# Optimization experiments

Hardware: AMD Instinct MI355X
Metric: run time of the kernel (lower is better)

The kernel has to match this reference:

```python
import jax, jax.numpy as jnp
import numpy as np

LN_EPS = 1e-3   # keras LayerNormalization default epsilon
EPS = 1e-5      # module's self.eps
QB = 128.0      # 2**(bits-1) with bits=8


def ste_round(x):
    # straight-through round: forward = round(x), backward = identity
    return x + jax.lax.stop_gradient(jnp.round(x) - x)


def setup_inputs() -> dict:
    key = jax.random.key(0)
    k1, k2 = jax.random.split(key)
    x = jax.random.normal(k1, (4, 8192, 1024), dtype=jnp.float32)
    weight = jax.random.normal(k2, (1024, 1024), dtype=jnp.float32) * 0.02
    ln_gamma = jnp.ones((1024,), dtype=jnp.float32)
    ln_beta = jnp.zeros((1024,), dtype=jnp.float32)
    return {"x": x, "weight": weight, "ln_gamma": ln_gamma, "ln_beta": ln_beta}


def reference(x, weight, ln_gamma, ln_beta):
    # LayerNorm over last axis (keras defaults: eps=1e-3, learnable scale/center)
    mu = jnp.mean(x, axis=-1, keepdims=True)
    var = jnp.var(x, axis=-1, keepdims=True)
    xn = (x - mu) * jax.lax.rsqrt(var + LN_EPS) * ln_gamma + ln_beta

    # 1.58-bit weight ternarization with STE round
    beta = jnp.mean(jnp.abs(weight))                     # per-tensor scale
    w_q = jnp.clip(ste_round(weight / (beta + EPS)), -1.0, 1.0)

    # activation quantization (flg_before_linear=True branch)
    gamma = jnp.max(jnp.abs(xn))                         # per-tensor absmax
    xq = jnp.clip(xn * QB / gamma, -QB + EPS, QB - EPS)

    # quantized matmul + fused rescale
    y = jnp.einsum('bsd,du->bsu', xq, w_q)
    return y * (gamma * beta / QB)
```

## Files before the change

kernel.cpp:

```cpp
#include <hip/hip_runtime.h>
#include <hip/hip_bf16.h>
#include <stdint.h>


#define M_ROWS 32768
#define KDIM 1024
#define NDIM 1024

typedef int   v4i  __attribute__((ext_vector_type(4)));
typedef int   v16i __attribute__((ext_vector_type(16)));

__device__ __forceinline__ void async16(const void* g, void* l) {
    __builtin_amdgcn_global_load_lds((const __attribute__((address_space(1))) uint32_t*)g,
                                     (__attribute__((address_space(3))) uint32_t*)l,
                                     16, 0, 0);
}

__global__ __launch_bounds__(256) void absum_k(const float* __restrict__ w,
                                               float* __restrict__ partials) {
    int idx = blockIdx.x * 256 + threadIdx.x;
    float4 v = ((const float4*)w)[idx];
    float s = fabsf(v.x) + fabsf(v.y) + fabsf(v.z) + fabsf(v.w);
    #pragma unroll
    for (int o = 32; o; o >>= 1) s += __shfl_xor(s, o);
    __shared__ float p[4];
    if ((threadIdx.x & 63) == 0) p[threadIdx.x >> 6] = s;
    __syncthreads();
    if (threadIdx.x == 0) partials[blockIdx.x] = p[0] + p[1] + p[2] + p[3];
}

__global__ __launch_bounds__(256) void quant_k(const float* __restrict__ w,
                                               const float* __restrict__ partials,
                                               char* __restrict__ wqT,
                                               float* __restrict__ wsum) {
    int t = threadIdx.x;
    float s = partials[t] + partials[t + 256] + partials[t + 512] + partials[t + 768];
    #pragma unroll
    for (int o = 32; o; o >>= 1) s += __shfl_xor(s, o);
    __shared__ float ps[4];
    if ((t & 63) == 0) ps[t >> 6] = s;
    __syncthreads();
    float total = ps[0] + ps[1] + ps[2] + ps[3];
    if (blockIdx.x == 0 && t == 0) wsum[0] = total;
    float beta = total * (1.0f / 1048576.0f);
    float inv  = 1.0f / (beta + 1e-5f);

    __shared__ char sT[64 * 80];
    int k0 = (blockIdx.x >> 4) * 64, n0 = (blockIdx.x & 15) * 64;
    int n_l = t & 63;
    #pragma unroll
    for (int r = 0; r < 16; ++r) {
        int k_l = (t >> 6) * 16 + r;
        float q = rintf(w[(size_t)(k0 + k_l) * NDIM + n0 + n_l] * inv);
        q = fminf(1.0f, fmaxf(-1.0f, q));
        sT[n_l * 80 + k_l] = (char)(int)q;
    }
    __syncthreads();
    int nn = t >> 2, c = t & 3;
    v4i val = *(const v4i*)&sT[nn * 80 + c * 16];
    *(v4i*)&wqT[(size_t)(n0 + nn) * KDIM + k0 + c * 16] = val;
}

__global__ __launch_bounds__(256) void ln_q_k(const float* __restrict__ x,
                                              const float* __restrict__ g,
                                              const float* __restrict__ b,
                                              char* __restrict__ xq,
                                              float* __restrict__ rscale) {
    int tid = threadIdx.x;
    int lane = tid & 63;
    int row = blockIdx.x * 4 + (tid >> 6);
    const float4* xr = (const float4*)(x + (size_t)row * KDIM);
    float4 v[4];
    #pragma unroll
    for (int j = 0; j < 4; ++j) v[j] = xr[lane + 64 * j];
    float s = 0.f, ss = 0.f;
    #pragma unroll
    for (int j = 0; j < 4; ++j) {
        s  += v[j].x + v[j].y + v[j].z + v[j].w;
        ss += v[j].x * v[j].x + v[j].y * v[j].y + v[j].z * v[j].z + v[j].w * v[j].w;
    }
    #pragma unroll
    for (int o = 32; o; o >>= 1) { s += __shfl_xor(s, o); ss += __shfl_xor(ss, o); }
    float mu  = s * (1.0f / 1024.0f);
    float var = ss * (1.0f / 1024.0f) - mu * mu;
    float rs  = rsqrtf(var + 1e-3f);
    float xn[16];
    float mx = 0.f;
    #pragma unroll
    for (int j = 0; j < 4; ++j) {
        int p = lane + 64 * j;
        float4 gg = ((const float4*)g)[p];
        float4 bb = ((const float4*)b)[p];
        xn[4*j+0] = (v[j].x - mu) * rs * gg.x + bb.x;
        xn[4*j+1] = (v[j].y - mu) * rs * gg.y + bb.y;
        xn[4*j+2] = (v[j].z - mu) * rs * gg.z + bb.z;
        xn[4*j+3] = (v[j].w - mu) * rs * gg.w + bb.w;
        #pragma unroll
        for (int e = 0; e < 4; ++e) mx = fmaxf(mx, fabsf(xn[4*j+e]));
    }
    #pragma unroll
    for (int o = 32; o; o >>= 1) mx = fmaxf(mx, __shfl_xor(mx, o));
    mx = fmaxf(mx, 1e-20f);
    float scl = mx * (1.0f / 127.0f);
    float inv = 127.0f / mx;
    if (lane == 0) rscale[row] = scl;
    #pragma unroll
    for (int j = 0; j < 4; ++j) {
        char4 c;
        c.x = (char)(int)rintf(xn[4*j+0] * inv);
        c.y = (char)(int)rintf(xn[4*j+1] * inv);
        c.z = (char)(int)rintf(xn[4*j+2] * inv);
        c.w = (char)(int)rintf(xn[4*j+3] * inv);
        *(char4*)(xq + (size_t)row * KDIM + (lane + 64 * j) * 4) = c;
    }
}

__global__ __launch_bounds__(256) void gemm_k(const char* __restrict__ A,
                                              const char* __restrict__ B,
                                              const float* __restrict__ wsum,
                                              const float* __restrict__ rscale,
                                              float* __restrict__ out) {
    __shared__ char sA[128 * 128];
    __shared__ char sB[128 * 128];
    int tid = threadIdx.x;
    int w = tid >> 6, lane = tid & 63;
    int half = lane >> 5, l31 = lane & 31;
    int wm = w & 1, wn = w >> 1;
    int xcd   = blockIdx.x & 7;
    int local = blockIdx.x >> 3;
    int bm0 = (xcd * 32 + (local >> 3)) * 128;
    int bn0 = (local & 7) * 128;

    v16i acc[2][2] = {};

    int r_sub = lane >> 3;
    int p     = lane & 7;

    for (int kt = 0; kt < 8; ++kt) {
        int k0 = kt * 128;
        #pragma unroll
        for (int t = 0; t < 4; ++t) {
            int rb  = w * 32 + t * 8;
            int row = rb + r_sub;
            int c   = p ^ (row & 7);
            async16(A + (size_t)(bm0 + row) * KDIM + k0 + c * 16, &sA[rb * 128]);
            async16(B + (size_t)(bn0 + row) * KDIM + k0 + c * 16, &sB[rb * 128]);
        }
        __syncthreads();
        #pragma unroll
        for (int kk = 0; kk < 4; ++kk) {
            v4i af[2], bf[2];
            int c16 = kk * 2 + half;
            #pragma unroll
            for (int i = 0; i < 2; ++i) {
                int m = wm * 64 + i * 32 + l31;
                af[i] = *(const v4i*)&sA[m * 128 + (c16 ^ (m & 7)) * 16];
                int n = wn * 64 + i * 32 + l31;
                bf[i] = *(const v4i*)&sB[n * 128 + (c16 ^ (n & 7)) * 16];
            }
            #pragma unroll
            for (int i = 0; i < 2; ++i)
                #pragma unroll
                for (int j = 0; j < 2; ++j)
                    acc[i][j] = __builtin_amdgcn_mfma_i32_32x32x32_i8(af[i], bf[j], acc[i][j], 0, 0, 0);
        }
        __syncthreads();
    }

    float beta = wsum[0] * (1.0f / 1048576.0f);
    #pragma unroll
    for (int i = 0; i < 2; ++i) {
        #pragma unroll
        for (int r = 0; r < 16; ++r) {
            int mrow = bm0 + wm * 64 + i * 32 + (r & 3) + 8 * (r >> 2) + 4 * half;
            float sc = rscale[mrow] * beta;
            #pragma unroll
            for (int j = 0; j < 2; ++j) {
                int ncol = bn0 + wn * 64 + j * 32 + l31;
                out[(size_t)mrow * NDIM + ncol] = (float)acc[i][j][r] * sc;
            }
        }
    }
}

extern "C" void kernel_launch(void* const* d_in, const int* in_sizes, int n_in,
                              void* d_out, int out_size, void* d_ws, size_t ws_size,
                              hipStream_t stream) {
    const float* x        = (const float*)d_in[0];
    const float* weight   = (const float*)d_in[1];
    const float* ln_gamma = (const float*)d_in[2];
    const float* ln_beta  = (const float*)d_in[3];
    float* out = (float*)d_out;

    float* wsum     = (float*)d_ws;
    float* partials = (float*)((char*)d_ws + 4096);
    float* rscale   = (float*)((char*)d_ws + 8192);
    char*  wqT      = (char*)d_ws + (1u << 18);
    char*  xq       = (char*)d_ws + (1u << 21);

    absum_k<<<1024, 256, 0, stream>>>(weight, partials);
    quant_k<<<256, 256, 0, stream>>>(weight, partials, wqT, wsum);
    ln_q_k<<<M_ROWS / 4, 256, 0, stream>>>(x, ln_gamma, ln_beta, xq, rscale);
    gemm_k<<<(M_ROWS / 128) * (NDIM / 128), 256, 0, stream>>>(xq, wqT, wsum, rscale, out);
}
```

Baseline: 274.0 us.

## Fuse LayerNorm-quantize into int8 GEMM with block-resident A and pre-tiled weights

The LayerNorm and activation quantization kernel is merged into the GEMM. Each 512-thread block quantizes 128 rows into a 128KB LDS tile and then computes all 1024 output columns from it, so the int8 activation buffer is never written to or read back from global memory. The weight quantizer now emits an MFMA-fragment-ordered layout, and B fragments are loaded directly from global/L2 without LDS staging. The trade-offs are a large LDS footprint (one block per CU, low occupancy), no overlap between the LN phase and the MFMA phase, and B reads that depend on L2/cache bandwidth.

```diff
diff --git a/kernel.cpp b/kernel.cpp
--- a/kernel.cpp
+++ b/kernel.cpp
@@ -1,5 +1,4 @@
 #include <hip/hip_runtime.h>
-#include <hip/hip_bf16.h>
 #include <stdint.h>
 
 
@@ -7,14 +6,8 @@
 #define KDIM 1024
 #define NDIM 1024
 
-typedef int   v4i  __attribute__((ext_vector_type(4)));
-typedef int   v16i __attribute__((ext_vector_type(16)));
-
-__device__ __forceinline__ void async16(const void* g, void* l) {
-    __builtin_amdgcn_global_load_lds((const __attribute__((address_space(1))) uint32_t*)g,
-                                     (__attribute__((address_space(3))) uint32_t*)l,
-                                     16, 0, 0);
-}
+typedef int v4i  __attribute__((ext_vector_type(4)));
+typedef int v16i __attribute__((ext_vector_type(16)));
 
 __global__ __launch_bounds__(256) void absum_k(const float* __restrict__ w,
                                                float* __restrict__ partials) {
@@ -31,7 +24,7 @@
 
 __global__ __launch_bounds__(256) void quant_k(const float* __restrict__ w,
                                                const float* __restrict__ partials,
-                                               char* __restrict__ wqT,
+                                               char* __restrict__ wqB,
                                                float* __restrict__ wsum) {
     int t = threadIdx.x;
     float s = partials[t] + partials[t + 256] + partials[t + 512] + partials[t + 768];
@@ -56,128 +49,117 @@
         sT[n_l * 80 + k_l] = (char)(int)q;
     }
     __syncthreads();
-    int nn = t >> 2, c = t & 3;
+    int nn = t & 63, c = t >> 6;
     v4i val = *(const v4i*)&sT[nn * 80 + c * 16];
-    *(v4i*)&wqT[(size_t)(n0 + nn) * KDIM + k0 + c * 16] = val;
+    int n = n0 + nn, k = k0 + c * 16;
+    size_t off = (size_t)(n >> 5) * 32768 + (size_t)(k >> 5) * 1024
+               + (size_t)((((k >> 4) & 1) * 32 + (n & 31)) * 16);
+    *(v4i*)&wqB[off] = val;
 }
 
-__global__ __launch_bounds__(256) void ln_q_k(const float* __restrict__ x,
-                                              const float* __restrict__ g,
-                                              const float* __restrict__ b,
-                                              char* __restrict__ xq,
-                                              float* __restrict__ rscale) {
+__global__ __launch_bounds__(512) void fused_k(const float* __restrict__ x,
+                                               const float* __restrict__ g,
+                                               const float* __restrict__ bia,
+                                               const char* __restrict__ wqB,
+                                               const float* __restrict__ wsum,
+                                               float* __restrict__ out) {
+    __shared__ char  sA[128 * 1024];
+    __shared__ float sRS[128];
     int tid = threadIdx.x;
-    int lane = tid & 63;
-    int row = blockIdx.x * 4 + (tid >> 6);
-    const float4* xr = (const float4*)(x + (size_t)row * KDIM);
-    float4 v[4];
-    #pragma unroll
-    for (int j = 0; j < 4; ++j) v[j] = xr[lane + 64 * j];
-    float s = 0.f, ss = 0.f;
+    int w = tid >> 6, lane = tid & 63;
+    int bm0 = blockIdx.x * 128;
+
+    float4 gg[4], bb[4];
     #pragma unroll
     for (int j = 0; j < 4; ++j) {
-        s  += v[j].x + v[j].y + v[j].z + v[j].w;
-        ss += v[j].x * v[j].x + v[j].y * v[j].y + v[j].z * v[j].z + v[j].w * v[j].w;
+        gg[j] = ((const float4*)g)[lane + 64 * j];
+        bb[j] = ((const float4*)bia)[lane + 64 * j];
     }
-    #pragma unroll
-    for (int o = 32; o; o >>= 1) { s += __shfl_xor(s, o); ss += __shfl_xor(ss, o); }
-    float mu  = s * (1.0f / 1024.0f);
-    float var = ss * (1.0f / 1024.0f) - mu * mu;
-    float rs  = rsqrtf(var + 1e-3f);
-    float xn[16];
-    float mx = 0.f;
-    #pragma unroll
-    for (int j = 0; j < 4; ++j) {
-        int p = lane + 64 * j;
-        float4 gg = ((const float4*)g)[p];
-        float4 bb = ((const float4*)b)[p];
-        xn[4*j+0] = (v[j].x - mu) * rs * gg.x + bb.x;
-        xn[4*j+1] = (v[j].y - mu) * rs * gg.y + bb.y;
-        xn[4*j+2] = (v[j].z - mu) * rs * gg.z + bb.z;
-        xn[4*j+3] = (v[j].w - mu) * rs * gg.w + bb.w;
+
+    #pragma unroll 2
+    for (int rr = 0; rr < 16; ++rr) {
+        int row = w * 16 + rr;
+        const float4* xr = (const float4*)(x + (size_t)(bm0 + row) * KDIM);
+        float4 v[4];
         #pragma unroll
-        for (int e = 0; e < 4; ++e) mx = fmaxf(mx, fabsf(xn[4*j+e]));
+        for (int j = 0; j < 4; ++j) v[j] = xr[lane + 64 * j];
+        float s = 0.f, ss = 0.f;
+        #pragma unroll
+        for (int j = 0; j < 4; ++j) {
+            s  += v[j].x + v[j].y + v[j].z + v[j].w;
+            ss += v[j].x * v[j].x + v[j].y * v[j].y + v[j].z * v[j].z + v[j].w * v[j].w;
+        }
+        #pragma unroll
+        for (int o = 32; o; o >>= 1) { s += __shfl_xor(s, o); ss += __shfl_xor(ss, o); }
+        float mu  = s * (1.0f / 1024.0f);
+        float var = ss * (1.0f / 1024.0f) - mu * mu;
+        float rs  = rsqrtf(var + 1e-3f);
+        float xn[16];
+        float mx = 0.f;
+        #pragma unroll
+        for (int j = 0; j < 4; ++j) {
+            xn[4*j+0] = (v[j].x - mu) * rs * gg[j].x + bb[j].x;
+            xn[4*j+1] = (v[j].y - mu) * rs * gg[j].y + bb[j].y;
+            xn[4*j+2] = (v[j].z - mu) * rs * gg[j].z + bb[j].z;
+            xn[4*j+3] = (v[j].w - mu) * rs * gg[j].w + bb[j].w;
+            #pragma unroll
+            for (int e = 0; e < 4; ++e) mx = fmaxf(mx, fabsf(xn[4*j+e]));
+        }
+        #pragma unroll
+        for (int o = 32; o; o >>= 1) mx = fmaxf(mx, __shfl_xor(mx, o));
+        mx = fmaxf(mx, 1e-20f);
+        if (lane == 0) sRS[row] = mx * (1.0f / 127.0f);
+        float inv = 127.0f / mx;
+        int sw = row & 7;
+        #pragma unroll
+        for (int j = 0; j < 4; ++j) {
+            char4 c;
+            c.x = (char)(int)rintf(xn[4*j+0] * inv);
+            c.y = (char)(int)rintf(xn[4*j+1] * inv);
+            c.z = (char)(int)rintf(xn[4*j+2] * inv);
+            c.w = (char)(int)rintf(xn[4*j+3] * inv);
+            int chunk = (lane >> 2) + 16 * j;
+            *(char4*)&sA[row * 1024 + ((chunk ^ sw) << 4) + ((lane & 3) << 2)] = c;
+        }
     }
-    #pragma unroll
-    for (int o = 32; o; o >>= 1) mx = fmaxf(mx, __shfl_xor(mx, o));
-    mx = fmaxf(mx, 1e-20f);
-    float scl = mx * (1.0f / 127.0f);
-    float inv = 127.0f / mx;
-    if (lane == 0) rscale[row] = scl;
-    #pragma unroll
-    for (int j = 0; j < 4; ++j) {
-        char4 c;
-        c.x = (char)(int)rintf(xn[4*j+0] * inv);
-        c.y = (char)(int)rintf(xn[4*j+1] * inv);
-        c.z = (char)(int)rintf(xn[4*j+2] * inv);
-        c.w = (char)(int)rintf(xn[4*j+3] * inv);
-        *(char4*)(xq + (size_t)row * KDIM + (lane + 64 * j) * 4) = c;
-    }
-}
+    __syncthreads();
 
-__global__ __launch_bounds__(256) void gemm_k(const char* __restrict__ A,
-                                              const char* __restrict__ B,
-                                              const float* __restrict__ wsum,
-                                              const float* __restrict__ rscale,
-                                              float* __restrict__ out) {
-    __shared__ char sA[128 * 128];
-    __shared__ char sB[128 * 128];
-    int tid = threadIdx.x;
-    int w = tid >> 6, lane = tid & 63;
-    int half = lane >> 5, l31 = lane & 31;
+    int l31 = lane & 31, half = lane >> 5;
     int wm = w & 1, wn = w >> 1;
-    int xcd   = blockIdx.x & 7;
-    int local = blockIdx.x >> 3;
-    int bm0 = (xcd * 32 + (local >> 3)) * 128;
-    int bn0 = (local & 7) * 128;
+    float beta = wsum[0] * (1.0f / 1048576.0f);
 
-    v16i acc[2][2] = {};
-
-    int r_sub = lane >> 3;
-    int p     = lane & 7;
-
-    for (int kt = 0; kt < 8; ++kt) {
-        int k0 = kt * 128;
-        #pragma unroll
-        for (int t = 0; t < 4; ++t) {
-            int rb  = w * 32 + t * 8;
-            int row = rb + r_sub;
-            int c   = p ^ (row & 7);
-            async16(A + (size_t)(bm0 + row) * KDIM + k0 + c * 16, &sA[rb * 128]);
-            async16(B + (size_t)(bn0 + row) * KDIM + k0 + c * 16, &sB[rb * 128]);
-        }
-        __syncthreads();
-        #pragma unroll
-        for (int kk = 0; kk < 4; ++kk) {
+    for (int bn = 0; bn < 4; ++bn) {
+        int n0 = bn * 256 + wn * 64;
+        const char* bp = wqB + (size_t)(n0 >> 5) * 32768 + lane * 16;
+        v16i acc[2][2] = {};
+        #pragma unroll 4
+        for (int kk = 0; kk < 32; ++kk) {
+            int c16 = kk * 2 + half;
             v4i af[2], bf[2];
-            int c16 = kk * 2 + half;
             #pragma unroll
             for (int i = 0; i < 2; ++i) {
                 int m = wm * 64 + i * 32 + l31;
-                af[i] = *(const v4i*)&sA[m * 128 + (c16 ^ (m & 7)) * 16];
-                int n = wn * 64 + i * 32 + l31;
-                bf[i] = *(const v4i*)&sB[n * 128 + (c16 ^ (n & 7)) * 16];
+                af[i] = *(const v4i*)&sA[m * 1024 + ((c16 ^ (m & 7)) << 4)];
             }
+            bf[0] = *(const v4i*)(bp + kk * 1024);
+            bf[1] = *(const v4i*)(bp + 32768 + kk * 1024);
             #pragma unroll
             for (int i = 0; i < 2; ++i)
                 #pragma unroll
                 for (int j = 0; j < 2; ++j)
                     acc[i][j] = __builtin_amdgcn_mfma_i32_32x32x32_i8(af[i], bf[j], acc[i][j], 0, 0, 0);
         }
-        __syncthreads();
-    }
-
-    float beta = wsum[0] * (1.0f / 1048576.0f);
-    #pragma unroll
-    for (int i = 0; i < 2; ++i) {
         #pragma unroll
-        for (int r = 0; r < 16; ++r) {
-            int mrow = bm0 + wm * 64 + i * 32 + (r & 3) + 8 * (r >> 2) + 4 * half;
-            float sc = rscale[mrow] * beta;
+        for (int i = 0; i < 2; ++i) {
             #pragma unroll
-            for (int j = 0; j < 2; ++j) {
-                int ncol = bn0 + wn * 64 + j * 32 + l31;
-                out[(size_t)mrow * NDIM + ncol] = (float)acc[i][j][r] * sc;
+            for (int r = 0; r < 16; ++r) {
+                int ml = wm * 64 + i * 32 + (r & 3) + 8 * (r >> 2) + 4 * half;
+                float sc = sRS[ml] * beta;
+                #pragma unroll
+                for (int j = 0; j < 2; ++j) {
+                    int nc = n0 + j * 32 + l31;
+                    out[(size_t)(bm0 + ml) * NDIM + nc] = (float)acc[i][j][r] * sc;
+                }
             }
         }
     }
@@ -194,12 +176,9 @@
 
     float* wsum     = (float*)d_ws;
     float* partials = (float*)((char*)d_ws + 4096);
-    float* rscale   = (float*)((char*)d_ws + 8192);
-    char*  wqT      = (char*)d_ws + (1u << 18);
-    char*  xq       = (char*)d_ws + (1u << 21);
+    char*  wqB      = (char*)d_ws + (1u << 18);
 
     absum_k<<<1024, 256, 0, stream>>>(weight, partials);
-    quant_k<<<256, 256, 0, stream>>>(weight, partials, wqT, wsum);
-    ln_q_k<<<M_ROWS / 4, 256, 0, stream>>>(x, ln_gamma, ln_beta, xq, rscale);
-    gemm_k<<<(M_ROWS / 128) * (NDIM / 128), 256, 0, stream>>>(xq, wqT, wsum, rscale, out);
+    quant_k<<<256, 256, 0, stream>>>(weight, partials, wqB, wsum);
+    fused_k<<<M_ROWS / 128, 512, 0, stream>>>(x, ln_gamma, ln_beta, wqB, wsum, out);
 }
```

Result: no change. 276.7 us (+1.0%).
